# Kernel optimization log

Hardware: AMD Instinct MI355X
Metric: run time of the kernel (lower is better)

The kernel has to match this reference:

```python
import jax, jax.numpy as jnp
import numpy as np

EPS = 1e-06
GEO_TEMP = 0.1
TOP_K = 32
ATTN_DIM = 256
CHANNELS = 1024
LN_EPS = 1e-05  # torch LayerNorm default


def _layernorm(x, g, b):
    mu = jnp.mean(x, axis=-1, keepdims=True)
    var = jnp.mean(jnp.square(x - mu), axis=-1, keepdims=True)
    return (x - mu) * jax.lax.rsqrt(var + LN_EPS) * g + b


def _flatten_rays(plucker):
    # plucker: [B,6,h,w] -> moments [B,N,3], dirs [B,N,3]
    b, _, h, w = plucker.shape
    rays = jnp.transpose(plucker, (0, 2, 3, 1)).reshape(b, h * w, 6)
    d = rays[..., :3]
    n = jnp.linalg.norm(d, axis=-1, keepdims=True)
    dirs = d / jnp.maximum(n, EPS)  # F.normalize semantics
    return rays[..., 3:], dirs


def _epipolar_bias(plucker_query, plucker_key):
    m_q, d_q = _flatten_rays(plucker_query)
    m_k, d_k = _flatten_rays(plucker_key)
    # reciprocal[b,i,j] = |d_q_i . m_k_j + d_k_j . m_q_i|
    reciprocal = jnp.abs(jnp.einsum('bic,bjc->bij', d_q, m_k) +
                         jnp.einsum('bjc,bic->bij', d_k, m_q))
    nq = jnp.linalg.norm(m_q, axis=-1)[:, :, None]  # [B,N,1]
    nk = jnp.linalg.norm(m_k, axis=-1)[:, None, :]  # [B,1,N]
    reciprocal = reciprocal / (nq + nk + EPS)
    geo_bias = -reciprocal / GEO_TEMP
    B, N, _ = geo_bias.shape
    if 0 < TOP_K < N:
        # keep the TOP_K smallest reciprocal entries per query row
        _, keep = jax.lax.top_k(-reciprocal, TOP_K)  # [B,N,K]
        b_idx = jnp.arange(B)[:, None, None]
        n_idx = jnp.arange(N)[None, :, None]
        drop = jnp.ones((B, N, N), dtype=bool).at[b_idx, n_idx, keep].set(False)
        geo_bias = jnp.where(drop, jnp.float32(-10000.0), geo_bias)
    return geo_bias


def setup_inputs() -> dict:
    key = jax.random.key(0)
    ks = jax.random.split(key, 12)
    B, C, h, w = 4, CHANNELS, 48, 48
    D = ATTN_DIM
    inp = {
        'query_map': jax.random.normal(ks[0], (B, C, h, w), jnp.float32),
        'key_value_map': jax.random.normal(ks[1], (B, C, h, w), jnp.float32),
        'plucker_query': jax.random.normal(ks[2], (B, 6, h, w), jnp.float32),
        'plucker_key': jax.random.normal(ks[3], (B, 6, h, w), jnp.float32),
        'ln_q_g': jnp.ones((C,), jnp.float32), 'ln_q_b': jnp.zeros((C,), jnp.float32),
        'ln_k_g': jnp.ones((C,), jnp.float32), 'ln_k_b': jnp.zeros((C,), jnp.float32),
        'Wq': jax.random.normal(ks[4], (D, C), jnp.float32) * (C ** -0.5),
        'bq': jnp.zeros((D,), jnp.float32),
        'Wk': jax.random.normal(ks[5], (D, C), jnp.float32) * (C ** -0.5),
        'bk': jnp.zeros((D,), jnp.float32),
        'Wv': jax.random.normal(ks[6], (D, C), jnp.float32) * (C ** -0.5),
        'bv': jnp.zeros((D,), jnp.float32),
        # NOTE: module zero-inits out_proj; randomized here for a non-trivial baseline
        'Wo': jax.random.normal(ks[7], (C, D), jnp.float32) * (D ** -0.5),
        'bo': jnp.zeros((C,), jnp.float32),
    }
    return inp


def reference(query_map, key_value_map, plucker_query, plucker_key,
              ln_q_g, ln_q_b, ln_k_g, ln_k_b,
              Wq, bq, Wk, bk, Wv, bv, Wo, bo):
    b, c, h, w = query_map.shape
    scale = ATTN_DIM ** (-0.5)
    # [B,C,H,W] -> [B,N,C]
    q_tokens = jnp.transpose(query_map.reshape(b, c, h * w), (0, 2, 1))
    kv_tokens = jnp.transpose(key_value_map.reshape(b, c, h * w), (0, 2, 1))
    q = _layernorm(q_tokens, ln_q_g, ln_q_b) @ Wq.T + bq
    k = _layernorm(kv_tokens, ln_k_g, ln_k_b) @ Wk.T + bk
    v = kv_tokens @ Wv.T + bv
    logits = jnp.einsum('bid,bjd->bij', q, k) * scale
    logits = logits + _epipolar_bias(plucker_query, plucker_key)
    attn = jax.nn.softmax(logits, axis=-1)
    fused = jnp.einsum('bij,bjd->bid', attn, v) @ Wo.T + bo  # [B,N,C]
    return jnp.transpose(fused, (0, 2, 1)).reshape(b, c, h, w)
```

## Files before the change

kernel.cpp:

```cpp
#include <hip/hip_runtime.h>

typedef unsigned short u16;
typedef unsigned int u32;
typedef unsigned long long u64;
typedef _Float16 f16;
typedef __attribute__((ext_vector_type(8))) _Float16 half8;
typedef __attribute__((ext_vector_type(4))) float f32x4;

#define HW 2304
#define CC 1024
#define DD 256
#define NB 4
#define CANDCAP 256
#define RANKC 33
#define GATE 0.099f

__device__ __forceinline__ float mul_s(float a, float b) {
  float r; asm("v_mul_f32 %0, %1, %2" : "=v"(r) : "v"(a), "v"(b)); return r;
}
__device__ __forceinline__ float add_s(float a, float b) {
  float r; asm("v_add_f32 %0, %1, %2" : "=v"(r) : "v"(a), "v"(b)); return r;
}
__device__ __forceinline__ void split16(float a, u16& hi, u16& lo) {
  f16 h = (f16)a;
  float hf = (float)h;
  f16 l = (f16)(a - hf);
  __builtin_memcpy(&hi, &h, 2);
  __builtin_memcpy(&lo, &l, 2);
}

__global__ void prep_weights(const float* __restrict__ wq, const float* __restrict__ wk,
                             const float* __restrict__ wv, const float* __restrict__ wo,
                             u16* __restrict__ qh, u16* __restrict__ ql,
                             u16* __restrict__ kh, u16* __restrict__ kl,
                             u16* __restrict__ vh, u16* __restrict__ vl,
                             u16* __restrict__ oh, u16* __restrict__ ol) {
  int idx = blockIdx.x * 256 + threadIdx.x;
  for (int i = idx; i < 4 * 262144; i += 262144) {
    int which = i >> 18, loc = i & 262143;
    const float* s = (which == 0) ? wq : (which == 1) ? wk : (which == 2) ? wv : wo;
    u16* dh = (which == 0) ? qh : (which == 1) ? kh : (which == 2) ? vh : oh;
    u16* dl = (which == 0) ? ql : (which == 1) ? kl : (which == 2) ? vl : ol;
    u16 h, l; split16(s[loc], h, l);
    dh[loc] = h; dl[loc] = l;
  }
}

__global__ void prep_rays(const float* __restrict__ pq, const float* __restrict__ pk,
                          float* __restrict__ qray, float* __restrict__ kray) {
#pragma clang fp contract(off)
  int t = blockIdx.x * 256 + threadIdx.x;
  const float* src = blockIdx.y ? pk : pq;
  float* dst = blockIdx.y ? kray : qray;
  int b = t / HW, i = t % HW;
  const float* sp = src + (size_t)b * 6 * HW + i;
  float d0 = sp[0], d1 = sp[HW], d2 = sp[2 * HW];
  float m0 = sp[3 * HW], m1 = sp[4 * HW], m2 = sp[5 * HW];
  float nd = __fsqrt_rn(add_s(add_s(mul_s(d0, d0), mul_s(d1, d1)), mul_s(d2, d2)));
  float nc = fmaxf(nd, 1e-6f);
  float ix = d0 / nc, iy = d1 / nc, iz = d2 / nc;
  float nm = __fsqrt_rn(add_s(add_s(mul_s(m0, m0), mul_s(m1, m1)), mul_s(m2, m2)));
  float4* dp = (float4*)(dst + (size_t)t * 12);
  dp[0] = make_float4(m0, m1, m2, nm);
  dp[1] = make_float4(ix, iy, iz, 0.f);
  dp[2] = make_float4(d0, d1, d2, 0.f);
}

__global__ __launch_bounds__(256) void ln_stats(const float* __restrict__ qmap,
                                                const float* __restrict__ kvmap,
                                                float* __restrict__ mu_q, float* __restrict__ rs_q,
                                                float* __restrict__ mu_k, float* __restrict__ rs_k) {
  const float* src = blockIdx.z ? kvmap : qmap;
  float* mu = blockIdx.z ? mu_k : mu_q;
  float* rs = blockIdx.z ? rs_k : rs_q;
  int b = blockIdx.y;
  int i0 = blockIdx.x * 32;
  int lane = threadIdx.x & 31, strip = threadIdx.x >> 5;
  const float* p = src + (size_t)b * CC * HW + i0 + lane;
  float s = 0.f, s2 = 0.f;
  for (int c = strip; c < CC; c += 8) {
    float v = p[(size_t)c * HW];
    s += v; s2 += v * v;
  }
  __shared__ float rsum[8][32], rsq[8][32];
  rsum[strip][lane] = s; rsq[strip][lane] = s2;
  __syncthreads();
  if (threadIdx.x < 32) {
    float ts = 0.f, tq = 0.f;
    for (int k = 0; k < 8; ++k) { ts += rsum[k][lane]; tq += rsq[k][lane]; }
    float m = ts * (1.f / 1024.f);
    float var = fmaxf(tq * (1.f / 1024.f) - m * m, 0.f);
    mu[b * HW + i0 + lane] = m;
    rs[b * HW + i0 + lane] = rsqrtf(var + 1e-5f);
  }
}

__global__ __launch_bounds__(256) void proj_mfma(
    const float* __restrict__ qmap, const float* __restrict__ kvmap,
    const float* __restrict__ gq, const float* __restrict__ bgq,
    const float* __restrict__ gk, const float* __restrict__ bgk,
    const u16* __restrict__ wqh, const u16* __restrict__ wql,
    const u16* __restrict__ wkh, const u16* __restrict__ wkl,
    const u16* __restrict__ wvh, const u16* __restrict__ wvl,
    const float* __restrict__ bq, const float* __restrict__ bk, const float* __restrict__ bv,
    const float* __restrict__ muq, const float* __restrict__ rsq,
    const float* __restrict__ muk, const float* __restrict__ rsk,
    float* __restrict__ qf, float* __restrict__ kf, float* __restrict__ vf) {
  int mtile = blockIdx.x, proj = blockIdx.y, b = blockIdx.z;
  int i0 = mtile * 64;
  const float* A; const u16* Wh; const u16* Wl;
  const float* gamma; const float* beta; const float* mup; const float* rsp; const float* bias;
  float* outp;
  if (proj == 0)      { A = qmap;  Wh = wqh; Wl = wql; gamma = gq; beta = bgq; mup = muq; rsp = rsq; bias = bq; outp = qf; }
  else if (proj == 1) { A = kvmap; Wh = wkh; Wl = wkl; gamma = gk; beta = bgk; mup = muk; rsp = rsk; bias = bk; outp = kf; }
  else                { A = kvmap; Wh = wvh; Wl = wvl; gamma = nullptr; beta = nullptr; mup = nullptr; rsp = nullptr; bias = bv; outp = vf; }
  __shared__ u16 Ah[64 * 72], Al[64 * 72];
  __shared__ float mul[64], rsl[64];
  int tid = threadIdx.x;
  int lane = tid & 63, wid = tid >> 6;
  if (proj < 2 && tid < 64) {
    mul[tid] = mup[b * HW + i0 + tid];
    rsl[tid] = rsp[b * HW + i0 + tid];
  }
  __syncthreads();
  f32x4 acc[4][4] = {};
  int c_loc = tid >> 2;
  int i4 = (tid & 3) * 4;
  int rowA = lane & 15, kch = (lane >> 4) * 8;
  for (int ks = 0; ks < 16; ++ks) {
    int c0 = ks * 64;
    float gma = 1.f, bet = 0.f;
    if (proj < 2) { gma = gamma[c0 + c_loc]; bet = beta[c0 + c_loc]; }
    const float* ap = A + ((size_t)(b * CC + c0 + c_loc)) * HW + i0;
#pragma unroll
    for (int p = 0; p < 4; ++p) {
      int ib = p * 16 + i4;
      float4 v = *(const float4*)(ap + ib);
      float e0 = v.x, e1 = v.y, e2 = v.z, e3 = v.w;
      if (proj < 2) {
        e0 = (e0 - mul[ib + 0]) * rsl[ib + 0] * gma + bet;
        e1 = (e1 - mul[ib + 1]) * rsl[ib + 1] * gma + bet;
        e2 = (e2 - mul[ib + 2]) * rsl[ib + 2] * gma + bet;
        e3 = (e3 - mul[ib + 3]) * rsl[ib + 3] * gma + bet;
      }
      u16 h, l;
      split16(e0, h, l); Ah[(ib + 0) * 72 + c_loc] = h; Al[(ib + 0) * 72 + c_loc] = l;
      split16(e1, h, l); Ah[(ib + 1) * 72 + c_loc] = h; Al[(ib + 1) * 72 + c_loc] = l;
      split16(e2, h, l); Ah[(ib + 2) * 72 + c_loc] = h; Al[(ib + 2) * 72 + c_loc] = l;
      split16(e3, h, l); Ah[(ib + 3) * 72 + c_loc] = h; Al[(ib + 3) * 72 + c_loc] = l;
    }
    __syncthreads();
#pragma unroll
    for (int kk = 0; kk < 2; ++kk) {
      int ko = kk * 32 + kch;
      half8 ah[4], al[4], bh[4], bl[4];
#pragma unroll
      for (int mf = 0; mf < 4; ++mf) {
        ah[mf] = *(const half8*)&Ah[(mf * 16 + rowA) * 72 + ko];
        al[mf] = *(const half8*)&Al[(mf * 16 + rowA) * 72 + ko];
      }
#pragma unroll
      for (int nf = 0; nf < 4; ++nf) {
        size_t woff = (size_t)(wid * 64 + nf * 16 + rowA) * CC + c0 + ko;
        bh[nf] = *(const half8*)&Wh[woff];
        bl[nf] = *(const half8*)&Wl[woff];
      }
#pragma unroll
      for (int mf = 0; mf < 4; ++mf)
#pragma unroll
        for (int nf = 0; nf < 4; ++nf) {
          acc[mf][nf] = __builtin_amdgcn_mfma_f32_16x16x32_f16(ah[mf], bh[nf], acc[mf][nf], 0, 0, 0);
          acc[mf][nf] = __builtin_amdgcn_mfma_f32_16x16x32_f16(ah[mf], bl[nf], acc[mf][nf], 0, 0, 0);
          acc[mf][nf] = __builtin_amdgcn_mfma_f32_16x16x32_f16(al[mf], bh[nf], acc[mf][nf], 0, 0, 0);
        }
    }
    __syncthreads();
  }
  int r4 = (lane >> 4) * 4, cold = lane & 15;
#pragma unroll
  for (int nf = 0; nf < 4; ++nf) {
    int dcol = wid * 64 + nf * 16 + cold;
    float bsv = bias[dcol];
#pragma unroll
    for (int mf = 0; mf < 4; ++mf) {
#pragma unroll
      for (int r = 0; r < 4; ++r) {
        int irow = i0 + mf * 16 + r4 + r;
        outp[(size_t)(b * HW + irow) * DD + dcol] = acc[mf][nf][r] + bsv;
      }
    }
  }
}

__global__ __launch_bounds__(64) void attn_f32(
    const float* __restrict__ qf, const float* __restrict__ kf, const float* __restrict__ vf,
    const float* __restrict__ qray, const float* __restrict__ kray,
    float* __restrict__ fusedf, float* __restrict__ dfused, int* __restrict__ flags) {
#pragma clang fp contract(off)
  int i = blockIdx.x, b = blockIdx.y;
  int lane = threadIdx.x;
  __shared__ u32 hist[1024];
  __shared__ float qs[DD];
  __shared__ int kidx[RANKC];
  __shared__ float kr[RANKC];
  __shared__ float lgt[RANKC];
  __shared__ float wgt[RANKC];
  __shared__ float dw[RANKC];
  __shared__ int cidx[CANDCAP];
  __shared__ float cr[CANDCAP];
  __shared__ int s_alt, s_last, s_hedge;
  int tok = b * HW + i;
  ((float4*)qs)[lane] = ((const float4*)(qf + (size_t)tok * DD))[lane];
  const float* qp = qray + (size_t)tok * 12;
  float4 mq = ((const float4*)qp)[0];
  float4 dq = ((const float4*)qp)[1];
#pragma unroll
  for (int k = 0; k < 16; ++k) hist[lane * 16 + k] = 0;
  __syncthreads();
  const float* krb = kray + (size_t)b * HW * 12;
  auto rcomp = [&](int j) -> float {
    const float4* kp4 = (const float4*)(krb + (size_t)j * 12);
    float4 km = kp4[0], kd = kp4[1];
    float p0 = mul_s(dq.x, km.x), p1 = mul_s(dq.y, km.y), p2 = mul_s(dq.z, km.z);
    float s1 = add_s(add_s(p0, p2), p1);
    float q0 = mul_s(kd.x, mq.x), q1 = mul_s(kd.y, mq.y), q2 = mul_s(kd.z, mq.z);
    float s2 = add_s(add_s(q0, q2), q1);
    float num = fabsf(add_s(s1, s2));
    float den = add_s(add_s(mq.w, km.w), 1e-6f);
    return num / den;
  };
  float rreg[36];
#pragma unroll
  for (int t = 0; t < 36; ++t) {
    rreg[t] = rcomp(t * 64 + lane);
    atomicAdd(&hist[__float_as_uint(rreg[t]) >> 22], 1u);
  }
  __syncthreads();
  int own = 0;
#pragma unroll
  for (int k = 0; k < 16; ++k) own += (int)hist[lane * 16 + k];
  int incl = own;
  for (int off = 1; off < 64; off <<= 1) {
    int nn = __shfl_up(incl, off);
    if (lane >= off) incl += nn;
  }
  u64 bal = __ballot(incl >= RANKC);
  int srcl = __ffsll((long long)bal) - 1;
  int exclv = __shfl(incl - own, srcl);
  int bstar = -1, below = 0, cum = exclv;
  for (int k = 0; k < 16; ++k) {
    int cnt = (int)hist[srcl * 16 + k];
    if (bstar < 0 && cum + cnt >= RANKC) { bstar = srcl * 16 + k; below = cum; }
    cum += cnt;
  }
  int kc = 0, ccn = 0;
#pragma unroll
  for (int t = 0; t < 36; ++t) {
    int j = t * 64 + lane;
    float r = rreg[t];
    int bin = (int)(__float_as_uint(r) >> 22);
    bool isk = bin < bstar, isc = bin == bstar;
    u64 bkm = __ballot(isk);
    u64 bcm = __ballot(isc);
    u64 mymask = (1ull << lane) - 1ull;
    if (isk) { int p = kc + __popcll(bkm & mymask); kidx[p] = j; kr[p] = r; }
    if (isc) { int p = ccn + __popcll(bcm & mymask); if (p < CANDCAP) { cidx[p] = j; cr[p] = r; } }
    kc += (int)__popcll(bkm);
    ccn += (int)__popcll(bcm);
  }
  __syncthreads();
  int m = RANKC - below;
  bool usec = (ccn <= CANDCAP);
  for (int s = 0; s < m; ++s) {
    float bvv = 3.402823466e38f; int bj = 0x7fffffff; int bp = -1;
    if (usec) {
      for (int p = lane; p < ccn; p += 64) {
        float v = cr[p]; int j = cidx[p];
        if (v < bvv || (v == bvv && j < bj)) { bvv = v; bj = j; bp = p; }
      }
    } else {
      for (int t = 0; t < 36; ++t) {
        int j = t * 64 + lane;
        float v = rcomp(j);
        if ((int)(__float_as_uint(v) >> 22) != bstar) continue;
        bool used = false;
        for (int u = 0; u < s; ++u) if (kidx[below + u] == j) { used = true; break; }
        if (!used && (v < bvv || (v == bvv && j < bj))) { bvv = v; bj = j; bp = -1; }
      }
    }
#pragma unroll
    for (int off = 32; off; off >>= 1) {
      float ov = __shfl_xor(bvv, off); int oj = __shfl_xor(bj, off); int op = __shfl_xor(bp, off);
      if (ov < bvv || (ov == bvv && oj < bj)) { bvv = ov; bj = oj; bp = op; }
    }
    if (lane == 0) {
      kidx[below + s] = bj; kr[below + s] = bvv;
      if (bp >= 0) cr[bp] = 3.402823466e38f;
    }
    __syncthreads();
  }
  if (lane == 0) {
    int ia = -1, ib = -1;
    for (int t = 0; t < RANKC; ++t) {
      bool gA = (ia < 0) || (kr[t] > kr[ia]) || (kr[t] == kr[ia] && kidx[t] > kidx[ia]);
      if (gA) { ib = ia; ia = t; }
      else {
        bool gB = (ib < 0) || (kr[t] > kr[ib]) || (kr[t] == kr[ib] && kidx[t] > kidx[ib]);
        if (gB) ib = t;
      }
    }
    float tau = 0.f;
    for (int u = 0; u < 2; ++u) {
      int t = u ? ib : ia;
      const float* kp = krb + (size_t)kidx[t] * 12;
      float sp = fabsf(dq.x * kp[0]) + fabsf(dq.y * kp[1]) + fabsf(dq.z * kp[2])
               + fabsf(kp[4] * mq.x) + fabsf(kp[5] * mq.y) + fabsf(kp[6] * mq.z);
      float den = (mq.w + kp[3]) + 1e-6f;
      tau += 20.0f * 5.9604645e-08f * sp / den + 4e-7f * kr[t];
    }
    s_alt = ia; s_last = ib;
    s_hedge = ((kr[ia] - kr[ib]) < tau) ? 1 : 0;
  }
  __syncthreads();
  if (lane < RANKC) {
    const float* kp = kf + (size_t)(b * HW + kidx[lane]) * DD;
    float dot = 0.f;
#pragma unroll 8
    for (int d2 = 0; d2 < DD / 4; ++d2) {
      float4 k4 = ((const float4*)kp)[d2];
      float4 q4 = ((const float4*)qs)[d2];
      dot = fmaf(k4.x, q4.x, dot);
      dot = fmaf(k4.y, q4.y, dot);
      dot = fmaf(k4.z, q4.z, dot);
      dot = fmaf(k4.w, q4.w, dot);
    }
    lgt[lane] = dot * 0.0625f - kr[lane] / 0.1f;
  }
  __syncthreads();
  if (lane == 0) {
    int ia = s_alt, ib = s_last;
    float m1 = -3.402823466e38f;
    for (int t = 0; t < RANKC; ++t) if (t != ia) m1 = fmaxf(m1, lgt[t]);
    float z1 = 0.f;
    for (int t = 0; t < RANKC; ++t) {
      float e = (t == ia) ? 0.f : expf(lgt[t] - m1);
      wgt[t] = e; z1 += e;
    }
    float iz1 = 1.f / z1;
    for (int t = 0; t < RANKC; ++t) wgt[t] *= iz1;
    if (s_hedge) {
      float m2 = -3.402823466e38f;
      for (int t = 0; t < RANKC; ++t) if (t != ib) m2 = fmaxf(m2, lgt[t]);
      float z2 = 0.f;
      for (int t = 0; t < RANKC; ++t) {
        float e = (t == ib) ? 0.f : expf(lgt[t] - m2);
        dw[t] = e; z2 += e;
      }
      float iz2 = 1.f / z2;
      for (int t = 0; t < RANKC; ++t) dw[t] = wgt[t] - dw[t] * iz2;
    }
  }
  __syncthreads();
  float4 o = make_float4(0.f, 0.f, 0.f, 0.f);
  float4 od = make_float4(0.f, 0.f, 0.f, 0.f);
  const float* vb = vf + (size_t)b * HW * DD;
  int hedge = s_hedge;
  for (int tt = 0; tt < RANKC; ++tt) {
    float wv = wgt[tt]; int j = kidx[tt];
    float4 vv = *(const float4*)(vb + (size_t)j * DD + lane * 4);
    o.x = fmaf(wv, vv.x, o.x);
    o.y = fmaf(wv, vv.y, o.y);
    o.z = fmaf(wv, vv.z, o.z);
    o.w = fmaf(wv, vv.w, o.w);
    if (hedge) {
      float dv = dw[tt];
      od.x = fmaf(dv, vv.x, od.x);
      od.y = fmaf(dv, vv.y, od.y);
      od.z = fmaf(dv, vv.z, od.z);
      od.w = fmaf(dv, vv.w, od.w);
    }
  }
  *(float4*)(fusedf + (size_t)tok * DD + lane * 4) = o;
  if (hedge) *(float4*)(dfused + (size_t)tok * DD + lane * 4) = od;
  if (lane == 0) flags[tok] = hedge;
}

__global__ __launch_bounds__(256) void hedge_gate(
    const float* __restrict__ Wo, const int* __restrict__ flags,
    const float* __restrict__ dfused, float* __restrict__ fusedf) {
  int tok = blockIdx.x;
  if (!flags[tok]) return;
  __shared__ float dfl[DD];
  __shared__ float wmax[8];
  int tid = threadIdx.x;
  dfl[tid] = dfused[(size_t)tok * DD + tid];
  __syncthreads();
  float lmax = 0.f;
  for (int k = 0; k < 4; ++k) {
    int c = k * 256 + tid;
    const float* wr = Wo + (size_t)c * DD;
    float dot = 0.f;
#pragma unroll 8
    for (int d = 0; d < DD; d += 4) {
      float4 w4 = *(const float4*)(wr + d);
      float4 f4 = *(const float4*)(dfl + d);
      dot = fmaf(w4.x, f4.x, dot);
      dot = fmaf(w4.y, f4.y, dot);
      dot = fmaf(w4.z, f4.z, dot);
      dot = fmaf(w4.w, f4.w, dot);
    }
    lmax = fmaxf(lmax, fabsf(dot));
  }
#pragma unroll
  for (int off = 32; off; off >>= 1) lmax = fmaxf(lmax, __shfl_xor(lmax, off));
  if ((tid & 63) == 0) wmax[tid >> 6] = lmax;
  __syncthreads();
  if (tid == 0) wmax[4] = fmaxf(fmaxf(wmax[0], wmax[1]), fmaxf(wmax[2], wmax[3]));
  __syncthreads();
  if (wmax[4] <= GATE) {
    fusedf[(size_t)tok * DD + tid] -= 0.5f * dfl[tid];
  }
}

__global__ __launch_bounds__(256) void out_mfma(
    const u16* __restrict__ woh, const u16* __restrict__ wol,
    const float* __restrict__ fusedf, const float* __restrict__ bo,
    float* __restrict__ out) {
  int itile = blockIdx.x, ctile = blockIdx.y, b = blockIdx.z;
  int i0 = itile * 128, c0 = ctile * 128;
  __shared__ u16 Bh[128 * 72], Bl[128 * 72];
  int tid = threadIdx.x, lane = tid & 63, wid = tid >> 6;
  int wm = (wid >> 1) * 64, wn = (wid & 1) * 64;
  f32x4 acc[4][4] = {};
  int rowA = lane & 15, kch = (lane >> 4) * 8;
  for (int ks = 0; ks < 4; ++ks) {
    int d0 = ks * 64;
#pragma unroll
    for (int p = 0; p < 4; ++p) {
      int rr = p * 32 + (tid >> 3);
      int dc = (tid & 7) * 8;
      const float* fp = &fusedf[(size_t)(b * HW + i0 + rr) * DD + d0 + dc];
      float4 f0 = *(const float4*)fp;
      float4 f1 = *(const float4*)(fp + 4);
      u16 h, l;
      split16(f0.x, h, l); Bh[rr * 72 + dc + 0] = h; Bl[rr * 72 + dc + 0] = l;
      split16(f0.y, h, l); Bh[rr * 72 + dc + 1] = h; Bl[rr * 72 + dc + 1] = l;
      split16(f0.z, h, l); Bh[rr * 72 + dc + 2] = h; Bl[rr * 72 + dc + 2] = l;
      split16(f0.w, h, l); Bh[rr * 72 + dc + 3] = h; Bl[rr * 72 + dc + 3] = l;
      split16(f1.x, h, l); Bh[rr * 72 + dc + 4] = h; Bl[rr * 72 + dc + 4] = l;
      split16(f1.y, h, l); Bh[rr * 72 + dc + 5] = h; Bl[rr * 72 + dc + 5] = l;
      split16(f1.z, h, l); Bh[rr * 72 + dc + 6] = h; Bl[rr * 72 + dc + 6] = l;
      split16(f1.w, h, l); Bh[rr * 72 + dc + 7] = h; Bl[rr * 72 + dc + 7] = l;
    }
    __syncthreads();
#pragma unroll
    for (int kk = 0; kk < 2; ++kk) {
      int ko = kk * 32 + kch;
      half8 ah[4], al[4], bh[4], bl[4];
#pragma unroll
      for (int mf = 0; mf < 4; ++mf) {
        size_t woff = (size_t)(c0 + wm + mf * 16 + rowA) * DD + d0 + ko;
        ah[mf] = *(const half8*)&woh[woff];
        al[mf] = *(const half8*)&wol[woff];
      }
#pragma unroll
      for (int nf = 0; nf < 4; ++nf) {
        bh[nf] = *(const half8*)&Bh[(wn + nf * 16 + rowA) * 72 + ko];
        bl[nf] = *(const half8*)&Bl[(wn + nf * 16 + rowA) * 72 + ko];
      }
#pragma unroll
      for (int mf = 0; mf < 4; ++mf)
#pragma unroll
        for (int nf = 0; nf < 4; ++nf) {
          acc[mf][nf] = __builtin_amdgcn_mfma_f32_16x16x32_f16(ah[mf], bh[nf], acc[mf][nf], 0, 0, 0);
          acc[mf][nf] = __builtin_amdgcn_mfma_f32_16x16x32_f16(ah[mf], bl[nf], acc[mf][nf], 0, 0, 0);
          acc[mf][nf] = __builtin_amdgcn_mfma_f32_16x16x32_f16(al[mf], bh[nf], acc[mf][nf], 0, 0, 0);
        }
    }
    __syncthreads();
  }
  int r4 = (lane >> 4) * 4, cold = lane & 15;
#pragma unroll
  for (int mf = 0; mf < 4; ++mf) {
#pragma unroll
    for (int r = 0; r < 4; ++r) {
      int crow = c0 + wm + mf * 16 + r4 + r;
      float bsv = bo[crow];
#pragma unroll
      for (int nf = 0; nf < 4; ++nf) {
        int icol = i0 + wn + nf * 16 + cold;
        out[(size_t)(b * CC + crow) * HW + icol] = acc[mf][nf][r] + bsv;
      }
    }
  }
}

extern "C" void kernel_launch(void* const* d_in, const int* in_sizes, int n_in,
                              void* d_out, int out_size, void* d_ws, size_t ws_size,
                              hipStream_t stream) {
  (void)in_sizes; (void)n_in; (void)out_size; (void)ws_size;
  const float* qmap = (const float*)d_in[0];
  const float* kvmap = (const float*)d_in[1];
  const float* pq = (const float*)d_in[2];
  const float* pk = (const float*)d_in[3];
  const float* lnqg = (const float*)d_in[4];
  const float* lnqb = (const float*)d_in[5];
  const float* lnkg = (const float*)d_in[6];
  const float* lnkb = (const float*)d_in[7];
  const float* Wq = (const float*)d_in[8];
  const float* bq = (const float*)d_in[9];
  const float* Wk = (const float*)d_in[10];
  const float* bk = (const float*)d_in[11];
  const float* Wv = (const float*)d_in[12];
  const float* bv = (const float*)d_in[13];
  const float* Wo = (const float*)d_in[14];
  const float* bo = (const float*)d_in[15];
  float* out = (float*)d_out;
  char* w = (char*)d_ws;
  size_t off = 0;
  auto take = [&](size_t n) { char* p = w + off; off += (n + 511) & ~(size_t)511; return p; };
  u16* wq_h = (u16*)take((size_t)DD * CC * 2);
  u16* wq_l = (u16*)take((size_t)DD * CC * 2);
  u16* wk_h = (u16*)take((size_t)DD * CC * 2);
  u16* wk_l = (u16*)take((size_t)DD * CC * 2);
  u16* wv_h = (u16*)take((size_t)DD * CC * 2);
  u16* wv_l = (u16*)take((size_t)DD * CC * 2);
  u16* wo_h = (u16*)take((size_t)CC * DD * 2);
  u16* wo_l = (u16*)take((size_t)CC * DD * 2);
  float* qray = (float*)take((size_t)NB * HW * 12 * 4);
  float* kray = (float*)take((size_t)NB * HW * 12 * 4);
  float* mu_q = (float*)take((size_t)NB * HW * 4);
  float* rs_q = (float*)take((size_t)NB * HW * 4);
  float* mu_k = (float*)take((size_t)NB * HW * 4);
  float* rs_k = (float*)take((size_t)NB * HW * 4);
  float* qf = (float*)take((size_t)NB * HW * DD * 4);
  float* kf = (float*)take((size_t)NB * HW * DD * 4);
  float* vf = (float*)take((size_t)NB * HW * DD * 4);
  float* fusedf = (float*)take((size_t)NB * HW * DD * 4);
  float* dfused = (float*)take((size_t)NB * HW * DD * 4);
  int* flags = (int*)take((size_t)NB * HW * 4);

  prep_weights<<<dim3(1024), 256, 0, stream>>>(Wq, Wk, Wv, Wo, wq_h, wq_l, wk_h, wk_l,
                                               wv_h, wv_l, wo_h, wo_l);
  prep_rays<<<dim3(36, 2), 256, 0, stream>>>(pq, pk, qray, kray);
  ln_stats<<<dim3(72, NB, 2), 256, 0, stream>>>(qmap, kvmap, mu_q, rs_q, mu_k, rs_k);
  proj_mfma<<<dim3(36, 3, NB), 256, 0, stream>>>(qmap, kvmap, lnqg, lnqb, lnkg, lnkb,
                                                 wq_h, wq_l, wk_h, wk_l, wv_h, wv_l,
                                                 bq, bk, bv, mu_q, rs_q, mu_k, rs_k,
                                                 qf, kf, vf);
  attn_f32<<<dim3(HW, NB), 64, 0, stream>>>(qf, kf, vf, qray, kray, fusedf, dfused, flags);
  hedge_gate<<<dim3(NB * HW), 256, 0, stream>>>(Wo, flags, dfused, fusedf);
  out_mfma<<<dim3(18, 8, NB), 256, 0, stream>>>(wo_h, wo_l, fusedf, bo, out);
}
```

Before: 364.7 us.

## Parallelize candidate logits and softmax across wavefront lanes with shuffles; swizzle block order

The per-row q·k dot products for the 33 kept candidates are now computed cooperatively: all 64 lanes each load a float4 slice of the key row and reduce with xor-shuffles. Before, 33 lanes each walked a full 256-wide key row serially. The softmax and hedge-softmax that lane 0 ran serially now use wavefront shuffle reductions for max and sum. The block index is also swizzled across batches and rows, which changes the scheduling order and possibly cache locality. Summation order differs from before, which may shift the near-tie hedge results slightly.

```diff
diff --git a/kernel.cpp b/kernel.cpp
--- a/kernel.cpp
+++ b/kernel.cpp
@@ -197,10 +197,11 @@
     const float* __restrict__ qray, const float* __restrict__ kray,
     float* __restrict__ fusedf, float* __restrict__ dfused, int* __restrict__ flags) {
 #pragma clang fp contract(off)
-  int i = blockIdx.x, b = blockIdx.y;
+  int flat = blockIdx.y * HW + blockIdx.x;
+  int swz = (flat & 7) * ((NB * HW) / 8) + (flat >> 3);
+  int b = swz / HW, i = swz - b * HW;
   int lane = threadIdx.x;
   __shared__ u32 hist[1024];
-  __shared__ float qs[DD];
   __shared__ int kidx[RANKC];
   __shared__ float kr[RANKC];
   __shared__ float lgt[RANKC];
@@ -210,7 +211,7 @@
   __shared__ float cr[CANDCAP];
   __shared__ int s_alt, s_last, s_hedge;
   int tok = b * HW + i;
-  ((float4*)qs)[lane] = ((const float4*)(qf + (size_t)tok * DD))[lane];
+  float4 qreg = ((const float4*)(qf + (size_t)tok * DD))[lane];
   const float* qp = qray + (size_t)tok * 12;
   float4 mq = ((const float4*)qp)[0];
   float4 dq = ((const float4*)qp)[1];
@@ -322,49 +323,42 @@
     s_hedge = ((kr[ia] - kr[ib]) < tau) ? 1 : 0;
   }
   __syncthreads();
-  if (lane < RANKC) {
-    const float* kp = kf + (size_t)(b * HW + kidx[lane]) * DD;
-    float dot = 0.f;
-#pragma unroll 8
-    for (int d2 = 0; d2 < DD / 4; ++d2) {
-      float4 k4 = ((const float4*)kp)[d2];
-      float4 q4 = ((const float4*)qs)[d2];
-      dot = fmaf(k4.x, q4.x, dot);
-      dot = fmaf(k4.y, q4.y, dot);
-      dot = fmaf(k4.z, q4.z, dot);
-      dot = fmaf(k4.w, q4.w, dot);
-    }
-    lgt[lane] = dot * 0.0625f - kr[lane] / 0.1f;
-  }
-  __syncthreads();
-  if (lane == 0) {
-    int ia = s_alt, ib = s_last;
-    float m1 = -3.402823466e38f;
-    for (int t = 0; t < RANKC; ++t) if (t != ia) m1 = fmaxf(m1, lgt[t]);
-    float z1 = 0.f;
-    for (int t = 0; t < RANKC; ++t) {
-      float e = (t == ia) ? 0.f : expf(lgt[t] - m1);
-      wgt[t] = e; z1 += e;
-    }
-    float iz1 = 1.f / z1;
-    for (int t = 0; t < RANKC; ++t) wgt[t] *= iz1;
-    if (s_hedge) {
-      float m2 = -3.402823466e38f;
-      for (int t = 0; t < RANKC; ++t) if (t != ib) m2 = fmaxf(m2, lgt[t]);
-      float z2 = 0.f;
-      for (int t = 0; t < RANKC; ++t) {
-        float e = (t == ib) ? 0.f : expf(lgt[t] - m2);
-        dw[t] = e; z2 += e;
-      }
-      float iz2 = 1.f / z2;
-      for (int t = 0; t < RANKC; ++t) dw[t] = wgt[t] - dw[t] * iz2;
+  for (int t = 0; t < RANKC; ++t) {
+    int j = kidx[t];
+    float4 k4 = *(const float4*)(kf + (size_t)(b * HW + j) * DD + lane * 4);
+    float d = fmaf(k4.x, qreg.x, fmaf(k4.y, qreg.y, fmaf(k4.z, qreg.z, k4.w * qreg.w)));
+#pragma unroll
+    for (int off = 32; off; off >>= 1) d += __shfl_xor(d, off);
+    if (lane == 0) lgt[t] = d * 0.0625f - kr[t] / 0.1f;
+  }
+  __syncthreads();
+  int ia = s_alt, ib = s_last, hedge = s_hedge;
+  {
+    float lgt_l = (lane < RANKC) ? lgt[lane] : -3.402823466e38f;
+    float mv = (lane < RANKC && lane != ia) ? lgt_l : -3.402823466e38f;
+#pragma unroll
+    for (int off = 32; off; off >>= 1) mv = fmaxf(mv, __shfl_xor(mv, off));
+    float e1 = (lane < RANKC && lane != ia) ? expf(lgt_l - mv) : 0.f;
+    float z1 = e1;
+#pragma unroll
+    for (int off = 32; off; off >>= 1) z1 += __shfl_xor(z1, off);
+    float w1 = e1 / z1;
+    if (lane < RANKC) wgt[lane] = w1;
+    if (hedge) {
+      float mv2 = (lane < RANKC && lane != ib) ? lgt_l : -3.402823466e38f;
+#pragma unroll
+      for (int off = 32; off; off >>= 1) mv2 = fmaxf(mv2, __shfl_xor(mv2, off));
+      float e2 = (lane < RANKC && lane != ib) ? expf(lgt_l - mv2) : 0.f;
+      float z2 = e2;
+#pragma unroll
+      for (int off = 32; off; off >>= 1) z2 += __shfl_xor(z2, off);
+      if (lane < RANKC) dw[lane] = w1 - e2 / z2;
     }
   }
   __syncthreads();
   float4 o = make_float4(0.f, 0.f, 0.f, 0.f);
   float4 od = make_float4(0.f, 0.f, 0.f, 0.f);
   const float* vb = vf + (size_t)b * HW * DD;
-  int hedge = s_hedge;
   for (int tt = 0; tt < RANKC; ++tt) {
     float wv = wgt[tt]; int j = kidx[tt];
     float4 vv = *(const float4*)(vb + (size_t)j * DD + lane * 4);
```

Measured after the change: 381.3 us. +4.6%, slower.
